# Kernel tuning notes

Measured on AMD Instinct MI355X. Metric: run time of the kernel, lower is better.

## Reference

```python
import jax, jax.numpy as jnp
import numpy as np

N_QUBITS = 8
D_K = 64
B, S = 8, 1024


def _single_qubit_states(xang, theta):
    # xang: [B,S,n] values in [-1,1] (post-tanh); theta: [n,3] Rot params (phi, theta, omega)
    # state = RZ(omega) @ RY(th) @ RZ(phi) @ RY(pi*xang) |0>
    a = xang * jnp.pi
    c = jnp.cos(a * 0.5)          # [B,S,n]
    s = jnp.sin(a * 0.5)
    phi, th, om = theta[:, 0], theta[:, 1], theta[:, 2]   # each [n]
    ct = jnp.cos(th * 0.5)
    st = jnp.sin(th * 0.5)
    e_mpo = jnp.exp(-0.5j * (phi + om))   # e^{-i(phi+omega)/2}
    e_pmo = jnp.exp(0.5j * (phi - om))    # e^{+i(phi-omega)/2}
    amp0 = e_mpo * ct * c - e_pmo * st * s
    amp1 = jnp.conj(e_pmo) * st * c + jnp.conj(e_mpo) * ct * s
    return jnp.stack([amp0, amp1], axis=-1)   # [B,S,n,2] complex64


def setup_inputs() -> dict:
    key = jax.random.key(0)
    k1, k2, k3, k4 = jax.random.split(key, 4)
    x = jax.random.normal(k1, (B, S, D_K), dtype=jnp.float32)
    theta_q = jax.random.normal(k2, (N_QUBITS, 3), dtype=jnp.float32) * 0.1
    theta_k = jax.random.normal(k3, (N_QUBITS, 3), dtype=jnp.float32) * 0.1
    W_v = jax.random.normal(k4, (D_K, D_K), dtype=jnp.float32) / np.sqrt(D_K)
    b_v = jnp.zeros((D_K,), dtype=jnp.float32)
    return {"x": x, "theta_q": theta_q, "theta_k": theta_k, "W_v": W_v, "b_v": b_v}


def reference(x, theta_q, theta_k, W_v, b_v):
    n = theta_q.shape[0]
    xn = jnp.tanh(x[..., :n])                 # [B,S,n]
    qs = _single_qubit_states(xn, theta_q)    # [B,S,n,2]
    ks = _single_qubit_states(xn, theta_k)    # [B,S,n,2]
    # per-qubit overlap <q_i | k_j> for every (b, s, t) pair
    ov = jnp.einsum('bsnc,btnc->bstn', jnp.conj(qs), ks)  # [B,S,S,n] complex
    mag2 = jnp.real(ov) ** 2 + jnp.imag(ov) ** 2
    core = jnp.prod(mag2, axis=-1)            # |<psi_q|psi_k>|^2 = swap-test <Z>
    scores = (core + 1.0) * 0.5               # [B,S,S]
    attn = jax.nn.softmax(scores, axis=-1)
    values = x @ W_v.T + b_v                  # [B,S,D]
    out = jnp.einsum('bst,btd->bsd', attn, values)
    return out, attn
```

## Files before the change

### kernel.cpp

```cpp
#include <hip/hip_runtime.h>
#include <hip/hip_fp16.h>
#include <math.h>

#define NQ 8
#define DK 64
#define NB 8
#define NS 1024
#define RB 8

typedef _Float16 h2v __attribute__((ext_vector_type(2)));

__device__ __forceinline__ float fdot2h(unsigned qu, unsigned ku, float acc) {
#if defined(__has_builtin) && __has_builtin(__builtin_amdgcn_fdot2)
    union { unsigned u; h2v h; } a, b;
    a.u = qu; b.u = ku;
    return __builtin_amdgcn_fdot2(a.h, b.h, acc, false);
#else
    __half2 qh = *(__half2*)&qu, kh = *(__half2*)&ku;
    float2 qf = __half22float2(qh), kf = __half22float2(kh);
    return fmaf(qf.x, kf.x, fmaf(qf.y, kf.y, acc));
#endif
}

__global__ __launch_bounds__(256) void prep_kernel(
    const float* __restrict__ x,
    const float* __restrict__ theta_q,
    const float* __restrict__ theta_k,
    const float* __restrict__ Wv,
    const float* __restrict__ bv,
    __half* __restrict__ qdh, __half* __restrict__ kdh,
    float* __restrict__ values) {
    int bid = blockIdx.x;
    int tid = threadIdx.x;
    if (bid < 2048) {
        int t = bid * 4 + (tid >> 6);
        int d = tid & 63;
        const float4* xr = (const float4*)(x + (size_t)t * DK);
        const float4* wr = (const float4*)(Wv + (size_t)d * DK);
        float a0 = bv[d], a1 = 0.f, a2 = 0.f, a3 = 0.f;
#pragma unroll
        for (int j = 0; j < DK / 4; ++j) {
            float4 xv = xr[j], wv = wr[j];
            a0 = fmaf(xv.x, wv.x, a0);
            a1 = fmaf(xv.y, wv.y, a1);
            a2 = fmaf(xv.z, wv.z, a2);
            a3 = fmaf(xv.w, wv.w, a3);
        }
        values[(size_t)t * DK + d] = (a0 + a1) + (a2 + a3);
    } else {
        __shared__ float tt[2][NQ][6];
        if (tid < 16) {
            int side = tid >> 3, n = tid & 7;
            const float* thp = side ? theta_k : theta_q;
            float phi = thp[n * 3 + 0], th = thp[n * 3 + 1], om = thp[n * 3 + 2];
            float st, ct; __sincosf(0.5f * th, &st, &ct);
            float smpo, cmpo; __sincosf(0.5f * (phi + om), &smpo, &cmpo);
            float spmo, cpmo; __sincosf(0.5f * (phi - om), &spmo, &cpmo);
            tt[side][n][0] = ct;  tt[side][n][1] = st;
            tt[side][n][2] = cmpo; tt[side][n][3] = smpo;
            tt[side][n][4] = cpmo; tt[side][n][5] = spmo;
        }
        __syncthreads();

        int gid = (bid - 2048) * 256 + tid;
        int tok = gid >> 3;
        int n = gid & 7;
        float xin = x[(size_t)tok * DK + n];
        float ex = __expf(2.0f * xin);
        float xn = 1.0f - 2.0f / (ex + 1.0f);
        float s, c;
        __sincosf(xn * 1.57079632679489662f, &s, &c);

#pragma unroll
        for (int side = 0; side < 2; ++side) {
            float ct = tt[side][n][0], st = tt[side][n][1];
            float cmpo = tt[side][n][2], smpo = tt[side][n][3];
            float cpmo = tt[side][n][4], spmo = tt[side][n][5];
            float a = ct * c, b2 = st * s, cc = st * c, d2 = ct * s;
            float a0re =  cmpo * a - cpmo * b2;
            float a0im = -smpo * a - spmo * b2;
            float a1re =  cpmo * cc + cmpo * d2;
            float a1im = -spmo * cc + smpo * d2;
            float d0 = fmaf(a0re, a0re, a0im * a0im);
            float d1 = fmaf(a1re, a1re, a1im * a1im);
            float ur = fmaf(a1re, a0re, a1im * a0im);
            float ui = fmaf(a1im, a0re, -a1re * a0im);
            if (side == 0) {
                __half2* qp = (__half2*)(qdh + (size_t)tok * 32 + n * 4);
                qp[0] = __floats2half2_rn(d0, d1);
                qp[1] = __floats2half2_rn(ur, ui);
            } else {
                __half2* kp = (__half2*)(kdh + (size_t)tok * 32 + n * 4);
                kp[0] = __floats2half2_rn(d0, d1);
                kp[1] = __floats2half2_rn(2.f * ur, 2.f * ui);
            }
        }
    }
}

__global__ __launch_bounds__(256, 4) void attn_kernel(
    const __half* __restrict__ qdh, const __half* __restrict__ kdh,
    const float* __restrict__ values,
    float* __restrict__ out, float* __restrict__ attn) {
    __shared__ float e_lds[RB][NS];
    __shared__ float red_lds[4][RB];
    __shared__ float inv_lds[RB];

    int tid = threadIdx.x;
    int gr0 = blockIdx.x * RB;
    int b = gr0 >> 10;
    int w = tid >> 6, lane = tid & 63;

    const __half* kfb = kdh + (size_t)b * NS * 32;

    int t0 = w * 256;
    uint4 kv[4][4];
#pragma unroll
    for (int j = 0; j < 4; ++j) {
        const uint4* kp = (const uint4*)(kfb + (size_t)(t0 + j * 64 + lane) * 32);
        kv[j][0] = kp[0]; kv[j][1] = kp[1]; kv[j][2] = kp[2]; kv[j][3] = kp[3];
    }

    float sums[RB];
#pragma unroll
    for (int r = 0; r < RB; ++r) sums[r] = 0.f;

#pragma unroll
    for (int r = 0; r < RB; ++r) {
        const unsigned* qp = (const unsigned*)(qdh + (size_t)(gr0 + r) * 32);
        unsigned sq[16];
#pragma unroll
        for (int i = 0; i < 16; ++i) sq[i] = __builtin_amdgcn_readfirstlane(qp[i]);
#pragma unroll
        for (int j = 0; j < 4; ++j) {
            float m0 = fdot2h(sq[ 0], kv[j][0].x, fdot2h(sq[ 1], kv[j][0].y, 0.f));
            float m1 = fdot2h(sq[ 2], kv[j][0].z, fdot2h(sq[ 3], kv[j][0].w, 0.f));
            float m2 = fdot2h(sq[ 4], kv[j][1].x, fdot2h(sq[ 5], kv[j][1].y, 0.f));
            float m3 = fdot2h(sq[ 6], kv[j][1].z, fdot2h(sq[ 7], kv[j][1].w, 0.f));
            float m4 = fdot2h(sq[ 8], kv[j][2].x, fdot2h(sq[ 9], kv[j][2].y, 0.f));
            float m5 = fdot2h(sq[10], kv[j][2].z, fdot2h(sq[11], kv[j][2].w, 0.f));
            float m6 = fdot2h(sq[12], kv[j][3].x, fdot2h(sq[13], kv[j][3].y, 0.f));
            float m7 = fdot2h(sq[14], kv[j][3].z, fdot2h(sq[15], kv[j][3].w, 0.f));
            float core = ((m0 * m1) * (m2 * m3)) * ((m4 * m5) * (m6 * m7));
            float e = __expf(fmaf(core, 0.5f, 0.5f));
            e_lds[r][t0 + j * 64 + lane] = e;
            sums[r] += e;
        }
    }

#pragma unroll
    for (int r = 0; r < RB; ++r) {
#pragma unroll
        for (int m = 1; m < 64; m <<= 1) sums[r] += __shfl_xor(sums[r], m, 64);
    }
    if (lane == 0) {
#pragma unroll
        for (int r = 0; r < RB; ++r) red_lds[w][r] = sums[r];
    }
    __syncthreads();
    if (tid < RB)
        inv_lds[tid] = 1.f / (red_lds[0][tid] + red_lds[1][tid] + red_lds[2][tid] + red_lds[3][tid]);
    __syncthreads();

    float* ab = attn + (size_t)gr0 * NS;
#pragma unroll
    for (int r = 0; r < RB; ++r) {
        float4 e4 = *(const float4*)&e_lds[r][tid * 4];
        float iv = inv_lds[r];
        *(float4*)&ab[(size_t)r * NS + tid * 4] =
            make_float4(e4.x * iv, e4.y * iv, e4.z * iv, e4.w * iv);
    }

    int tg = tid >> 4, dg = tid & 15;
    const float* vb = values + (size_t)b * NS * DK;
    float acc[RB][4];
#pragma unroll
    for (int r = 0; r < RB; ++r) { acc[r][0] = acc[r][1] = acc[r][2] = acc[r][3] = 0.f; }

    for (int jj = 0; jj < 16; ++jj) {
        int t = jj * 64 + tg * 4;
        const float* vp = vb + (size_t)t * DK + dg * 4;
        float4 v0 = *(const float4*)(vp);
        float4 v1 = *(const float4*)(vp + DK);
        float4 v2 = *(const float4*)(vp + 2 * DK);
        float4 v3 = *(const float4*)(vp + 3 * DK);
#pragma unroll
        for (int r = 0; r < RB; ++r) {
            float4 e4 = *(const float4*)&e_lds[r][t];
            acc[r][0] = fmaf(e4.x, v0.x, fmaf(e4.y, v1.x, fmaf(e4.z, v2.x, fmaf(e4.w, v3.x, acc[r][0]))));
            acc[r][1] = fmaf(e4.x, v0.y, fmaf(e4.y, v1.y, fmaf(e4.z, v2.y, fmaf(e4.w, v3.y, acc[r][1]))));
            acc[r][2] = fmaf(e4.x, v0.z, fmaf(e4.y, v1.z, fmaf(e4.z, v2.z, fmaf(e4.w, v3.z, acc[r][2]))));
            acc[r][3] = fmaf(e4.x, v0.w, fmaf(e4.y, v1.w, fmaf(e4.z, v2.w, fmaf(e4.w, v3.w, acc[r][3]))));
        }
    }

    float* red = &e_lds[0][0];
#pragma unroll
    for (int h = 0; h < 2; ++h) {
        __syncthreads();
#pragma unroll
        for (int r = 0; r < 4; ++r) {
            *(float4*)&red[((size_t)tg * 4 + r) * 64 + dg * 4] =
                make_float4(acc[h * 4 + r][0], acc[h * 4 + r][1],
                            acc[h * 4 + r][2], acc[h * 4 + r][3]);
        }
        __syncthreads();
        int r2 = tid >> 6, d = tid & 63;
        float o = 0.f;
#pragma unroll
        for (int g = 0; g < 16; ++g) o += red[((size_t)g * 4 + r2) * 64 + d];
        out[((size_t)(gr0 + h * 4 + r2)) * DK + d] = o * inv_lds[h * 4 + r2];
    }
}

extern "C" void kernel_launch(void* const* d_in, const int* in_sizes, int n_in,
                              void* d_out, int out_size, void* d_ws, size_t ws_size,
                              hipStream_t stream) {
    const float* x       = (const float*)d_in[0];
    const float* theta_q = (const float*)d_in[1];
    const float* theta_k = (const float*)d_in[2];
    const float* W_v     = (const float*)d_in[3];
    const float* b_v     = (const float*)d_in[4];

    float* out  = (float*)d_out;
    float* attn = (float*)d_out + (size_t)NB * NS * DK;

    __half* qdh    = (__half*)d_ws;
    __half* kdh    = qdh + (size_t)NB * NS * 32;
    float*  values = (float*)(kdh + (size_t)NB * NS * 32);

    prep_kernel<<<2048 + NB * NS * NQ / 256, 256, 0, stream>>>(
        x, theta_q, theta_k, W_v, b_v, qdh, kdh, values);
    attn_kernel<<<NB * NS / RB, 256, 0, stream>>>(qdh, kdh, values, out, attn);
}
```

Before: 54.14 us.

## Use fp16 MFMA for attn@V with transposed half-precision values

Values are now stored transposed in fp16 ([B,D,S]), and the softmax numerators are kept in LDS as fp16 with a padded pitch. The attn@V product runs on MFMA 16x16x16 f16 instructions, one wave per 16-column slice of the output. Half of the 16 MFMA rows are duplicates because only 8 query rows are used. This drops the scalar FMA loop and the LDS cross-group reduction, and halves the values traffic and LDS footprint. The cost is lower precision: attn is now computed from fp16-rounded exponentials, and the values are also rounded to fp16.

Measured after the change: 66.66 us. 23.1% more time.

```diff
diff --git a/kernel.cpp b/kernel.cpp
--- a/kernel.cpp
+++ b/kernel.cpp
@@ -7,8 +7,11 @@
 #define NB 8
 #define NS 1024
 #define RB 8
+#define EPITCH 1032
 
 typedef _Float16 h2v __attribute__((ext_vector_type(2)));
+typedef _Float16 h4v __attribute__((ext_vector_type(4)));
+typedef float    f4v __attribute__((ext_vector_type(4)));
 
 __device__ __forceinline__ float fdot2h(unsigned qu, unsigned ku, float acc) {
 #if defined(__has_builtin) && __has_builtin(__builtin_amdgcn_fdot2)
@@ -29,7 +32,7 @@
     const float* __restrict__ Wv,
     const float* __restrict__ bv,
     __half* __restrict__ qdh, __half* __restrict__ kdh,
-    float* __restrict__ values) {
+    __half* __restrict__ vt) {
     int bid = blockIdx.x;
     int tid = threadIdx.x;
     if (bid < 2048) {
@@ -46,7 +49,9 @@
             a2 = fmaf(xv.z, wv.z, a2);
             a3 = fmaf(xv.w, wv.w, a3);
         }
-        values[(size_t)t * DK + d] = (a0 + a1) + (a2 + a3);
+        float v = (a0 + a1) + (a2 + a3);
+        int b = t >> 10, ti = t & 1023;
+        vt[(((size_t)(b * DK + d)) << 10) + ti] = __float2half_rn(v);
     } else {
         __shared__ float tt[2][NQ][6];
         if (tid < 16) {
@@ -100,9 +105,9 @@
 
 __global__ __launch_bounds__(256, 4) void attn_kernel(
     const __half* __restrict__ qdh, const __half* __restrict__ kdh,
-    const float* __restrict__ values,
+    const __half* __restrict__ vt,
     float* __restrict__ out, float* __restrict__ attn) {
-    __shared__ float e_lds[RB][NS];
+    __shared__ __align__(16) __half e16[RB][EPITCH];
     __shared__ float red_lds[4][RB];
     __shared__ float inv_lds[RB];
 
@@ -143,7 +148,7 @@
             float m7 = fdot2h(sq[14], kv[j][3].z, fdot2h(sq[15], kv[j][3].w, 0.f));
             float core = ((m0 * m1) * (m2 * m3)) * ((m4 * m5) * (m6 * m7));
             float e = __expf(fmaf(core, 0.5f, 0.5f));
-            e_lds[r][t0 + j * 64 + lane] = e;
+            e16[r][t0 + j * 64 + lane] = __float2half_rn(e);
             sums[r] += e;
         }
     }
@@ -165,52 +170,51 @@
     float* ab = attn + (size_t)gr0 * NS;
 #pragma unroll
     for (int r = 0; r < RB; ++r) {
-        float4 e4 = *(const float4*)&e_lds[r][tid * 4];
         float iv = inv_lds[r];
+        uint2 raw = *(const uint2*)&e16[r][tid * 4];
+        __half2* hp = (__half2*)&raw;
+        float2 lo = __half22float2(hp[0]), hi = __half22float2(hp[1]);
         *(float4*)&ab[(size_t)r * NS + tid * 4] =
-            make_float4(e4.x * iv, e4.y * iv, e4.z * iv, e4.w * iv);
-    }
-
-    int tg = tid >> 4, dg = tid & 15;
-    const float* vb = values + (size_t)b * NS * DK;
-    float acc[RB][4];
-#pragma unroll
-    for (int r = 0; r < RB; ++r) { acc[r][0] = acc[r][1] = acc[r][2] = acc[r][3] = 0.f; }
-
-    for (int jj = 0; jj < 16; ++jj) {
-        int t = jj * 64 + tg * 4;
-        const float* vp = vb + (size_t)t * DK + dg * 4;
-        float4 v0 = *(const float4*)(vp);
-        float4 v1 = *(const float4*)(vp + DK);
-        float4 v2 = *(const float4*)(vp + 2 * DK);
-        float4 v3 = *(const float4*)(vp + 3 * DK);
-#pragma unroll
-        for (int r = 0; r < RB; ++r) {
-            float4 e4 = *(const float4*)&e_lds[r][t];
-            acc[r][0] = fmaf(e4.x, v0.x, fmaf(e4.y, v1.x, fmaf(e4.z, v2.x, fmaf(e4.w, v3.x, acc[r][0]))));
-            acc[r][1] = fmaf(e4.x, v0.y, fmaf(e4.y, v1.y, fmaf(e4.z, v2.y, fmaf(e4.w, v3.y, acc[r][1]))));
-            acc[r][2] = fmaf(e4.x, v0.z, fmaf(e4.y, v1.z, fmaf(e4.z, v2.z, fmaf(e4.w, v3.z, acc[r][2]))));
-            acc[r][3] = fmaf(e4.x, v0.w, fmaf(e4.y, v1.w, fmaf(e4.z, v2.w, fmaf(e4.w, v3.w, acc[r][3]))));
-        }
-    }
-
-    float* red = &e_lds[0][0];
-#pragma unroll
-    for (int h = 0; h < 2; ++h) {
-        __syncthreads();
-#pragma unroll
-        for (int r = 0; r < 4; ++r) {
-            *(float4*)&red[((size_t)tg * 4 + r) * 64 + dg * 4] =
-                make_float4(acc[h * 4 + r][0], acc[h * 4 + r][1],
-                            acc[h * 4 + r][2], acc[h * 4 + r][3]);
-        }
-        __syncthreads();
-        int r2 = tid >> 6, d = tid & 63;
-        float o = 0.f;
-#pragma unroll
-        for (int g = 0; g < 16; ++g) o += red[((size_t)g * 4 + r2) * 64 + d];
-        out[((size_t)(gr0 + h * 4 + r2)) * DK + d] = o * inv_lds[h * 4 + r2];
-    }
+            make_float4(lo.x * iv, lo.y * iv, hi.x * iv, hi.y * iv);
+    }
+
+#if defined(__has_builtin) && __has_builtin(__builtin_amdgcn_mfma_f32_16x16x16f16)
+    {
+        int arow = lane & 15; if (arow >= RB) arow -= RB;
+        int kofs = (lane >> 4) * 4;
+        const __half* ap = &e16[arow][kofs];
+        const __half* bp = vt + (((size_t)(b * DK + w * 16 + (lane & 15))) << 10) + kofs;
+        f4v acc = {0.f, 0.f, 0.f, 0.f};
+#pragma unroll 4
+        for (int kt = 0; kt < 64; ++kt) {
+            h4v a = *(const h4v*)(ap + kt * 16);
+            h4v bb = *(const h4v*)(bp + kt * 16);
+            acc = __builtin_amdgcn_mfma_f32_16x16x16f16(a, bb, acc, 0, 0, 0);
+        }
+        if (lane < 32) {
+            int ccol = lane & 15;
+            int rbase = (lane >> 4) * 4;
+#pragma unroll
+            for (int reg = 0; reg < 4; ++reg) {
+                int row = rbase + reg;
+                out[((size_t)(gr0 + row)) * DK + w * 16 + ccol] = acc[reg] * inv_lds[row];
+            }
+        }
+    }
+#else
+    {
+        const __half* vtb = vt + (((size_t)b * DK) << 10);
+        for (int idx = tid; idx < RB * DK; idx += 256) {
+            int row = idx >> 6, d = idx & 63;
+            const __half* ep = &e16[row][0];
+            const __half* vp = vtb + ((size_t)d << 10);
+            float o = 0.f;
+            for (int t = 0; t < NS; ++t)
+                o = fmaf(__half2float(ep[t]), __half2float(vp[t]), o);
+            out[((size_t)(gr0 + row)) * DK + d] = o * inv_lds[row];
+        }
+    }
+#endif
 }
 
 extern "C" void kernel_launch(void* const* d_in, const int* in_sizes, int n_in,
@@ -225,11 +229,11 @@
     float* out  = (float*)d_out;
     float* attn = (float*)d_out + (size_t)NB * NS * DK;
 
-    __half* qdh    = (__half*)d_ws;
-    __half* kdh    = qdh + (size_t)NB * NS * 32;
-    float*  values = (float*)(kdh + (size_t)NB * NS * 32);
+    __half* qdh = (__half*)d_ws;
+    __half* kdh = qdh + (size_t)NB * NS * 32;
+    __half* vt  = kdh + (size_t)NB * NS * 32;
 
     prep_kernel<<<2048 + NB * NS * NQ / 256, 256, 0, stream>>>(
-        x, theta_q, theta_k, W_v, b_v, qdh, kdh, values);
-    attn_kernel<<<NB * NS / RB, 256, 0, stream>>>(qdh, kdh, values, out, attn);
-}
+        x, theta_q, theta_k, W_v, b_v, qdh, kdh, vt);
+    attn_kernel<<<NB * NS / RB, 256, 0, stream>>>(qdh, kdh, vt, out, attn);
+}
```

## Store values and exp scores in fp16 pairs and use dot2 for PV

Applied to the files above, without the earlier changes.

The values matrix is now written in half precision, interleaved in token pairs, and the exponentiated scores are kept in LDS as fp16. This lets the attention-times-values accumulation use packed fp16 dot2 instructions. Rows per block drop from 8 to 4, which doubles the grid and reloads K per block, and the loop order changes so each K vector is loaded once and reused across the query rows. The goal is less memory traffic and LDS use and fewer FMAs. The cost is extra fp16 rounding error in attn and out.

After: 51.50 us. -4.9%, faster.

```diff
diff --git a/kernel.cpp b/kernel.cpp
--- a/kernel.cpp
+++ b/kernel.cpp
@@ -6,7 +6,8 @@
 #define DK 64
 #define NB 8
 #define NS 1024
-#define RB 8
+#define RB 4
+#define EPITCH 1032
 
 typedef _Float16 h2v __attribute__((ext_vector_type(2)));
 
@@ -29,7 +30,7 @@
     const float* __restrict__ Wv,
     const float* __restrict__ bv,
     __half* __restrict__ qdh, __half* __restrict__ kdh,
-    float* __restrict__ values) {
+    __half* __restrict__ v2) {
     int bid = blockIdx.x;
     int tid = threadIdx.x;
     if (bid < 2048) {
@@ -46,7 +47,9 @@
             a2 = fmaf(xv.z, wv.z, a2);
             a3 = fmaf(xv.w, wv.w, a3);
         }
-        values[(size_t)t * DK + d] = (a0 + a1) + (a2 + a3);
+        float v = (a0 + a1) + (a2 + a3);
+        int b = t >> 10, ti = t & 1023;
+        v2[((size_t)(b * 512 + (ti >> 1)) * 64 + d) * 2 + (ti & 1)] = __float2half_rn(v);
     } else {
         __shared__ float tt[2][NQ][6];
         if (tid < 16) {
@@ -100,9 +103,11 @@
 
 __global__ __launch_bounds__(256, 4) void attn_kernel(
     const __half* __restrict__ qdh, const __half* __restrict__ kdh,
-    const float* __restrict__ values,
+    const __half* __restrict__ v2,
     float* __restrict__ out, float* __restrict__ attn) {
-    __shared__ float e_lds[RB][NS];
+    __shared__ __align__(16) unsigned char smem[16 * RB * 64 * 4];
+    __half (*e16)[EPITCH] = (__half(*)[EPITCH])smem;
+    float* red = (float*)smem;
     __shared__ float red_lds[4][RB];
     __shared__ float inv_lds[RB];
 
@@ -113,37 +118,37 @@
 
     const __half* kfb = kdh + (size_t)b * NS * 32;
 
+    unsigned sq[RB][16];
+#pragma unroll
+    for (int r = 0; r < RB; ++r) {
+        const unsigned* qp = (const unsigned*)(qdh + (size_t)(gr0 + r) * 32);
+#pragma unroll
+        for (int i = 0; i < 16; ++i) sq[r][i] = __builtin_amdgcn_readfirstlane(qp[i]);
+    }
+
+    float sums[RB];
+#pragma unroll
+    for (int r = 0; r < RB; ++r) sums[r] = 0.f;
+
     int t0 = w * 256;
-    uint4 kv[4][4];
 #pragma unroll
     for (int j = 0; j < 4; ++j) {
-        const uint4* kp = (const uint4*)(kfb + (size_t)(t0 + j * 64 + lane) * 32);
-        kv[j][0] = kp[0]; kv[j][1] = kp[1]; kv[j][2] = kp[2]; kv[j][3] = kp[3];
-    }
-
-    float sums[RB];
-#pragma unroll
-    for (int r = 0; r < RB; ++r) sums[r] = 0.f;
-
-#pragma unroll
-    for (int r = 0; r < RB; ++r) {
-        const unsigned* qp = (const unsigned*)(qdh + (size_t)(gr0 + r) * 32);
-        unsigned sq[16];
-#pragma unroll
-        for (int i = 0; i < 16; ++i) sq[i] = __builtin_amdgcn_readfirstlane(qp[i]);
-#pragma unroll
-        for (int j = 0; j < 4; ++j) {
-            float m0 = fdot2h(sq[ 0], kv[j][0].x, fdot2h(sq[ 1], kv[j][0].y, 0.f));
-            float m1 = fdot2h(sq[ 2], kv[j][0].z, fdot2h(sq[ 3], kv[j][0].w, 0.f));
-            float m2 = fdot2h(sq[ 4], kv[j][1].x, fdot2h(sq[ 5], kv[j][1].y, 0.f));
-            float m3 = fdot2h(sq[ 6], kv[j][1].z, fdot2h(sq[ 7], kv[j][1].w, 0.f));
-            float m4 = fdot2h(sq[ 8], kv[j][2].x, fdot2h(sq[ 9], kv[j][2].y, 0.f));
-            float m5 = fdot2h(sq[10], kv[j][2].z, fdot2h(sq[11], kv[j][2].w, 0.f));
-            float m6 = fdot2h(sq[12], kv[j][3].x, fdot2h(sq[13], kv[j][3].y, 0.f));
-            float m7 = fdot2h(sq[14], kv[j][3].z, fdot2h(sq[15], kv[j][3].w, 0.f));
+        int t = t0 + j * 64 + lane;
+        const uint4* kp = (const uint4*)(kfb + (size_t)t * 32);
+        uint4 k0 = kp[0], k1 = kp[1], k2 = kp[2], k3 = kp[3];
+#pragma unroll
+        for (int r = 0; r < RB; ++r) {
+            float m0 = fdot2h(sq[r][ 0], k0.x, fdot2h(sq[r][ 1], k0.y, 0.f));
+            float m1 = fdot2h(sq[r][ 2], k0.z, fdot2h(sq[r][ 3], k0.w, 0.f));
+            float m2 = fdot2h(sq[r][ 4], k1.x, fdot2h(sq[r][ 5], k1.y, 0.f));
+            float m3 = fdot2h(sq[r][ 6], k1.z, fdot2h(sq[r][ 7], k1.w, 0.f));
+            float m4 = fdot2h(sq[r][ 8], k2.x, fdot2h(sq[r][ 9], k2.y, 0.f));
+            float m5 = fdot2h(sq[r][10], k2.z, fdot2h(sq[r][11], k2.w, 0.f));
+            float m6 = fdot2h(sq[r][12], k3.x, fdot2h(sq[r][13], k3.y, 0.f));
+            float m7 = fdot2h(sq[r][14], k3.z, fdot2h(sq[r][15], k3.w, 0.f));
             float core = ((m0 * m1) * (m2 * m3)) * ((m4 * m5) * (m6 * m7));
             float e = __expf(fmaf(core, 0.5f, 0.5f));
-            e_lds[r][t0 + j * 64 + lane] = e;
+            e16[r][t] = __float2half_rn(e);
             sums[r] += e;
         }
     }
@@ -165,51 +170,48 @@
     float* ab = attn + (size_t)gr0 * NS;
 #pragma unroll
     for (int r = 0; r < RB; ++r) {
-        float4 e4 = *(const float4*)&e_lds[r][tid * 4];
         float iv = inv_lds[r];
+        uint2 raw = *(const uint2*)&e16[r][tid * 4];
+        __half2* hp = (__half2*)&raw;
+        float2 lo = __half22float2(hp[0]), hi = __half22float2(hp[1]);
         *(float4*)&ab[(size_t)r * NS + tid * 4] =
-            make_float4(e4.x * iv, e4.y * iv, e4.z * iv, e4.w * iv);
+            make_float4(lo.x * iv, lo.y * iv, hi.x * iv, hi.y * iv);
     }
 
     int tg = tid >> 4, dg = tid & 15;
-    const float* vb = values + (size_t)b * NS * DK;
+    const __half* v2b = v2 + (size_t)b * 512 * 128;
     float acc[RB][4];
 #pragma unroll
     for (int r = 0; r < RB; ++r) { acc[r][0] = acc[r][1] = acc[r][2] = acc[r][3] = 0.f; }
 
-    for (int jj = 0; jj < 16; ++jj) {
-        int t = jj * 64 + tg * 4;
-        const float* vp = vb + (size_t)t * DK + dg * 4;
-        float4 v0 = *(const float4*)(vp);
-        float4 v1 = *(const float4*)(vp + DK);
-        float4 v2 = *(const float4*)(vp + 2 * DK);
-        float4 v3 = *(const float4*)(vp + 3 * DK);
+    for (int jj = 0; jj < 32; ++jj) {
+        int p = jj * 16 + tg;
+        uint4 vv = *(const uint4*)(v2b + (size_t)p * 128 + dg * 8);
+        unsigned ep[RB];
+#pragma unroll
+        for (int r = 0; r < RB; ++r) ep[r] = *(const unsigned*)&e16[r][2 * p];
 #pragma unroll
         for (int r = 0; r < RB; ++r) {
-            float4 e4 = *(const float4*)&e_lds[r][t];
-            acc[r][0] = fmaf(e4.x, v0.x, fmaf(e4.y, v1.x, fmaf(e4.z, v2.x, fmaf(e4.w, v3.x, acc[r][0]))));
-            acc[r][1] = fmaf(e4.x, v0.y, fmaf(e4.y, v1.y, fmaf(e4.z, v2.y, fmaf(e4.w, v3.y, acc[r][1]))));
-            acc[r][2] = fmaf(e4.x, v0.z, fmaf(e4.y, v1.z, fmaf(e4.z, v2.z, fmaf(e4.w, v3.z, acc[r][2]))));
-            acc[r][3] = fmaf(e4.x, v0.w, fmaf(e4.y, v1.w, fmaf(e4.z, v2.w, fmaf(e4.w, v3.w, acc[r][3]))));
-        }
-    }
-
-    float* red = &e_lds[0][0];
-#pragma unroll
-    for (int h = 0; h < 2; ++h) {
-        __syncthreads();
-#pragma unroll
-        for (int r = 0; r < 4; ++r) {
-            *(float4*)&red[((size_t)tg * 4 + r) * 64 + dg * 4] =
-                make_float4(acc[h * 4 + r][0], acc[h * 4 + r][1],
-                            acc[h * 4 + r][2], acc[h * 4 + r][3]);
-        }
-        __syncthreads();
+            acc[r][0] = fdot2h(ep[r], vv.x, acc[r][0]);
+            acc[r][1] = fdot2h(ep[r], vv.y, acc[r][1]);
+            acc[r][2] = fdot2h(ep[r], vv.z, acc[r][2]);
+            acc[r][3] = fdot2h(ep[r], vv.w, acc[r][3]);
+        }
+    }
+
+    __syncthreads();
+#pragma unroll
+    for (int r = 0; r < RB; ++r) {
+        *(float4*)&red[((size_t)tg * RB + r) * 64 + dg * 4] =
+            make_float4(acc[r][0], acc[r][1], acc[r][2], acc[r][3]);
+    }
+    __syncthreads();
+    {
         int r2 = tid >> 6, d = tid & 63;
         float o = 0.f;
 #pragma unroll
-        for (int g = 0; g < 16; ++g) o += red[((size_t)g * 4 + r2) * 64 + d];
-        out[((size_t)(gr0 + h * 4 + r2)) * DK + d] = o * inv_lds[h * 4 + r2];
+        for (int g = 0; g < 16; ++g) o += red[((size_t)g * RB + r2) * 64 + d];
+        out[((size_t)(gr0 + r2)) * DK + d] = o * inv_lds[r2];
     }
 }
 
@@ -225,11 +227,11 @@
     float* out  = (float*)d_out;
     float* attn = (float*)d_out + (size_t)NB * NS * DK;
 
-    __half* qdh    = (__half*)d_ws;
-    __half* kdh    = qdh + (size_t)NB * NS * 32;
-    float*  values = (float*)(kdh + (size_t)NB * NS * 32);
+    __half* qdh = (__half*)d_ws;
+    __half* kdh = qdh + (size_t)NB * NS * 32;
+    __half* v2  = kdh + (size_t)NB * NS * 32;
 
     prep_kernel<<<2048 + NB * NS * NQ / 256, 256, 0, stream>>>(
-        x, theta_q, theta_k, W_v, b_v, qdh, kdh, values);
-    attn_kernel<<<NB * NS / RB, 256, 0, stream>>>(qdh, kdh, values, out, attn);
-}
+        x, theta_q, theta_k, W_v, b_v, qdh, kdh, v2);
+    attn_kernel<<<NB * NS / RB, 256, 0, stream>>>(qdh, kdh, v2, out, attn);
+}
```
